# Performance work log

Measured on AMD Instinct MI355X. Metric: run time of the kernel, lower is better.

The kernel has to match this reference:

```python
import jax, jax.numpy as jnp
import numpy as np

B, T, C = 4, 2048, 2048
H, KV, HD = 16, 4, 128  # n_head, n_kv_head, head_dim
G = H // KV             # query heads per kv head


def _rope(t, cos, sin):
    # t: [B, T, h, HD]; cos/sin: [T, HD//2] -> broadcast as [1, T, 1, HD//2]
    tr = t.reshape(t.shape[:-1] + (HD // 2, 2))
    t_r, t_i = tr[..., 0], tr[..., 1]
    c = cos[None, :, None, :]
    s = sin[None, :, None, :]
    o_r = t_r * c - t_i * s
    o_i = t_r * s + t_i * c
    return jnp.stack((o_r, o_i), axis=-1).reshape(t.shape)


def setup_inputs() -> dict:
    key = jax.random.key(0)
    ks = jax.random.split(key, 7)
    sc = 0.02
    return {
        "x": jax.random.normal(ks[0], (B, T, C), jnp.float32),
        "cos_freqs": jnp.cos(jnp.outer(jnp.arange(T, dtype=jnp.float32),
                                       1.0 / (10000.0 ** (jnp.arange(HD // 2, dtype=jnp.float32) * 2 / HD)))),
        "sin_freqs": jnp.sin(jnp.outer(jnp.arange(T, dtype=jnp.float32),
                                       1.0 / (10000.0 ** (jnp.arange(HD // 2, dtype=jnp.float32) * 2 / HD)))),
        "wq": jax.random.normal(ks[1], (H * HD, C), jnp.float32) * sc,
        "wk": jax.random.normal(ks[2], (KV * HD, C), jnp.float32) * sc,
        "wv": jax.random.normal(ks[3], (KV * HD, C), jnp.float32) * sc,
        "wo": jax.random.normal(ks[4], (C, H * HD), jnp.float32) * sc,
    }


def reference(x, cos_freqs, sin_freqs, wq, wk, wv, wo):
    # projections (Linear with bias=False: y = x @ W.T)
    q = (x @ wq.T).reshape(B, T, H, HD)
    k = (x @ wk.T).reshape(B, T, KV, HD)
    v = (x @ wv.T).reshape(B, T, KV, HD)
    q, k = _rope(q, cos_freqs, sin_freqs), _rope(k, cos_freqs, sin_freqs)
    # GQA attention without materializing repeated K/V: group q heads per kv head
    qg = q.reshape(B, T, KV, G, HD).transpose(0, 2, 3, 1, 4)  # [B,KV,G,T,HD]
    kh = k.transpose(0, 2, 1, 3)                              # [B,KV,T,HD]
    vh = v.transpose(0, 2, 1, 3)                              # [B,KV,T,HD]
    scale = 1.0 / jnp.sqrt(jnp.float32(HD))
    scores = jnp.einsum('bkgtd,bksd->bkgts', qg, kh) * scale  # [B,KV,G,T,T]
    mask = jnp.tril(jnp.ones((T, T), dtype=bool))
    scores = jnp.where(mask, scores, jnp.float32(-jnp.inf))
    attn = jax.nn.softmax(scores, axis=-1)
    out = jnp.einsum('bkgts,bksd->bkgtd', attn, vh)           # [B,KV,G,T,HD]
    out = out.transpose(0, 3, 1, 2, 4).reshape(B, T, H * HD)
    return out @ wo.T
```

## Files before the change

### kernel.cpp

```cpp
#include <hip/hip_runtime.h>
#include <hip/hip_bf16.h>
#include <math.h>

typedef __attribute__((ext_vector_type(8))) short short8;
typedef __attribute__((ext_vector_type(4))) float floatx4;

__device__ __forceinline__ float bf2f(unsigned short u) {
  union { unsigned int i; float f; } x; x.i = ((unsigned int)u) << 16; return x.f;
}
__device__ __forceinline__ unsigned short f2bf(float f) {
  union { float f; unsigned int i; } x; x.f = f;
  unsigned int r = x.i + 0x7FFFu + ((x.i >> 16) & 1u);
  return (unsigned short)(r >> 16);
}
__device__ __forceinline__ unsigned int pack2bf(float a, float b) {
  return (unsigned int)f2bf(a) | ((unsigned int)f2bf(b) << 16);
}
__device__ __forceinline__ void gl16(const void* g, void* l) {
  __builtin_amdgcn_global_load_lds(
      (const __attribute__((address_space(1))) unsigned int*)g,
      (__attribute__((address_space(3))) unsigned int*)l, 16, 0, 0);
}
#define BARF  do { __builtin_amdgcn_s_barrier(); asm volatile("" ::: "memory"); } while (0)

__global__ void cvt_f32_bf16(const float* __restrict__ in, unsigned short* __restrict__ out, int n4) {
  int i = blockIdx.x * blockDim.x + threadIdx.x;
  if (i >= n4) return;
  float4 v = ((const float4*)in)[i];
  ushort4 o;
  o.x = f2bf(v.x); o.y = f2bf(v.y); o.z = f2bf(v.z); o.w = f2bf(v.w);
  ((ushort4*)out)[i] = o;
}

template<int MODE>
__global__ __launch_bounds__(512, 2) void gemm_bt(const unsigned short* __restrict__ A,
                                                  const unsigned short* __restrict__ Bw,
                                                  void* __restrict__ out0,
                                                  unsigned short* __restrict__ vtg,
                                                  int M, int N, int K, int nbx) {
  extern __shared__ unsigned short SM[];
  const int nb = gridDim.x;
  const int bid = blockIdx.x;
  const int tile = (bid & 7) * (nb >> 3) + (bid >> 3);
  const int n0 = (tile % nbx) * 256, m0 = (tile / nbx) * 256;
  const int tid = threadIdx.x;
  const int lane = tid & 63, wave = tid >> 6;
  const int wm = wave >> 2, wn = wave & 3;
  const int r = lane & 15, g = lane >> 4;
  const int rh = r >> 1;
  const int slot = (((r & 1) << 2) | g) ^ rh;

  const int sg8 = (tid & 7) ^ ((tid >> 3) & 7);
  const int srow = 2 * (tid >> 3) + (sg8 >> 2);
  const int scol = (sg8 & 3) * 8;
  const unsigned short* Agb = A  + (size_t)(m0 + srow) * K + scol;
  const unsigned short* Bgb = Bw + (size_t)(n0 + srow) * K + scol;
  const size_t K128 = (size_t)K * 128;
  char* const SMb = (char*)SM;

  const int aob = (wm * 64 + rh) * 64 + slot * 8;
  const int bob = 16384 + (wn * 32 + rh) * 64 + slot * 8;

  auto STA = [&](int s, int t, int kh) {
    const unsigned short* gp = Agb + ((size_t)t << 6) + kh * 32;
    char* d = SMb + s * 65536 + kh * 16384 + wave * 1024;
    gl16(gp,        d);
    gl16(gp + K128, d + 8192);
  };
  auto STB = [&](int s, int t, int kh) {
    const unsigned short* gp = Bgb + ((size_t)t << 6) + kh * 32;
    char* d = SMb + s * 65536 + 32768 + kh * 16384 + wave * 1024;
    gl16(gp,        d);
    gl16(gp + K128, d + 8192);
  };

  floatx4 acc[8][4] = {};
  const int NT = K >> 6;

  STA(0, 0, 0); STB(0, 0, 0);
  STA(0, 0, 1); STB(0, 0, 1);
  asm volatile("s_waitcnt vmcnt(4)" ::: "memory");
  BARF;

  for (int t = 0; t < NT; ++t) {
    const int s = t & 1;
    const unsigned short* Ls = SM + s * 32768;
    const bool pf = (t + 1 < NT);
    short8 bfr[4], af[4];

#pragma unroll
    for (int j = 0; j < 4; ++j) bfr[j] = *(const short8*)&Ls[bob + j * 512];
#pragma unroll
    for (int i = 0; i < 4; ++i) af[i] = *(const short8*)&Ls[aob + i * 512];
    if (pf) STA(s ^ 1, t + 1, 0);
    BARF;
    __builtin_amdgcn_s_setprio(1);
#pragma unroll
    for (int i = 0; i < 4; ++i)
#pragma unroll
      for (int j = 0; j < 4; ++j)
        acc[i][j] = __builtin_amdgcn_mfma_f32_16x16x32_bf16(af[i], bfr[j], acc[i][j], 0, 0, 0);
    __builtin_amdgcn_s_setprio(0);
    BARF;

#pragma unroll
    for (int i = 0; i < 4; ++i) af[i] = *(const short8*)&Ls[aob + (4 + i) * 512];
    if (pf) {
      STB(s ^ 1, t + 1, 0);
      asm volatile("s_waitcnt vmcnt(4)" ::: "memory");
    } else {
      asm volatile("s_waitcnt vmcnt(0)" ::: "memory");
    }
    BARF;
    __builtin_amdgcn_s_setprio(1);
#pragma unroll
    for (int i = 0; i < 4; ++i)
#pragma unroll
      for (int j = 0; j < 4; ++j)
        acc[4 + i][j] = __builtin_amdgcn_mfma_f32_16x16x32_bf16(af[i], bfr[j], acc[4 + i][j], 0, 0, 0);
    __builtin_amdgcn_s_setprio(0);
    BARF;

#pragma unroll
    for (int j = 0; j < 4; ++j) bfr[j] = *(const short8*)&Ls[bob + 8192 + j * 512];
#pragma unroll
    for (int i = 0; i < 4; ++i) af[i] = *(const short8*)&Ls[aob + 8192 + i * 512];
    if (pf) STA(s ^ 1, t + 1, 1);
    BARF;
    __builtin_amdgcn_s_setprio(1);
#pragma unroll
    for (int i = 0; i < 4; ++i)
#pragma unroll
      for (int j = 0; j < 4; ++j)
        acc[i][j] = __builtin_amdgcn_mfma_f32_16x16x32_bf16(af[i], bfr[j], acc[i][j], 0, 0, 0);
    __builtin_amdgcn_s_setprio(0);
    BARF;

#pragma unroll
    for (int i = 0; i < 4; ++i) af[i] = *(const short8*)&Ls[aob + 8192 + (4 + i) * 512];
    if (pf) {
      STB(s ^ 1, t + 1, 1);
      asm volatile("s_waitcnt vmcnt(4)" ::: "memory");
    }
    BARF;
    __builtin_amdgcn_s_setprio(1);
#pragma unroll
    for (int i = 0; i < 4; ++i)
#pragma unroll
      for (int j = 0; j < 4; ++j)
        acc[4 + i][j] = __builtin_amdgcn_mfma_f32_16x16x32_bf16(af[i], bfr[j], acc[4 + i][j], 0, 0, 0);
    __builtin_amdgcn_s_setprio(0);
    BARF;
  }

  if (MODE == 0) {
    float* SMf = (float*)SM;
    float* outp = (float*)out0;
#pragma unroll
    for (int sp = 0; sp < 4; ++sp) {
      __syncthreads();
      if (wn == sp) {
#pragma unroll
        for (int i = 0; i < 8; ++i)
#pragma unroll
          for (int j = 0; j < 4; ++j)
#pragma unroll
            for (int q = 0; q < 4; ++q)
              SMf[(wm * 128 + i * 16 + g * 4 + q) * 64 + j * 16 + r] = acc[i][j][q];
      }
      __syncthreads();
#pragma unroll
      for (int it = 0; it < 8; ++it) {
        int c = it * 512 + tid;
        int ml = c >> 4, c4 = c & 15;
        float4 v = *(float4*)&SMf[ml * 64 + c4 * 4];
        *(float4*)(outp + (size_t)(m0 + ml) * N + n0 + sp * 64 + c4 * 4) = v;
      }
    }
  } else if (n0 < 2560) {
    unsigned short* outp = (unsigned short*)out0;
#pragma unroll
    for (int sp = 0; sp < 2; ++sp) {
      __syncthreads();
      if (wm == sp) {
#pragma unroll
        for (int i = 0; i < 8; ++i)
#pragma unroll
          for (int j = 0; j < 4; ++j)
#pragma unroll
            for (int q = 0; q < 4; ++q)
              SM[(i * 16 + g * 4 + q) * 256 + wn * 64 + j * 16 + r] = f2bf(acc[i][j][q]);
      }
      __syncthreads();
#pragma unroll
      for (int it = 0; it < 8; ++it) {
        int c = it * 512 + tid;
        int ml = c >> 5, c8 = c & 31;
        short8 v = *(short8*)&SM[ml * 256 + c8 * 8];
        *(short8*)(outp + (size_t)(m0 + sp * 128 + ml) * N + n0 + c8 * 8) = v;
      }
    }
  } else {
#pragma unroll
    for (int sp = 0; sp < 8; ++sp) {
      __syncthreads();
      if (wave == sp) {
#pragma unroll
        for (int i = 0; i < 8; ++i)
#pragma unroll
          for (int j = 0; j < 4; ++j)
#pragma unroll
            for (int q = 0; q < 4; ++q) {
              int ml = i * 16 + g * 4 + q;
              int nl = j * 16 + r;
              SM[nl * 128 + (((ml >> 3) ^ (nl & 7)) << 3) + (ml & 7)] = f2bf(acc[i][j][q]);
            }
      }
      __syncthreads();
#pragma unroll
      for (int it = 0; it < 2; ++it) {
        int c = it * 512 + tid;
        int nl = c >> 4, m8 = c & 15;
        short8 v = *(short8*)&SM[nl * 128 + ((m8 ^ (nl & 7)) << 3)];
        *(short8*)(vtg + (size_t)(n0 - 2560 + (sp & 3) * 64 + nl) * 8192 + m0 + (sp >> 2) * 128 + m8 * 8) = v;
      }
    }
  }
}

__global__ void rope_inplace(unsigned short* __restrict__ t,
                             const float* __restrict__ cosf, const float* __restrict__ sinf,
                             int heads, int rowStride, int total, float scale) {
  int i = blockIdx.x * blockDim.x + threadIdx.x;
  if (i >= total) return;
  int d8 = i & 15;
  int rem = i >> 4;
  int head = rem % heads;
  int tok = rem / heads;
  int tpos = tok & 2047;
  unsigned short* p = t + (size_t)tok * rowStride + head * 128 + d8 * 8;
  short8 v = *(short8*)p;
  float4 c = *(const float4*)(cosf + (size_t)tpos * 64 + d8 * 4);
  float4 s = *(const float4*)(sinf + (size_t)tpos * 64 + d8 * 4);
  float cc[4] = {c.x, c.y, c.z, c.w};
  float ss[4] = {s.x, s.y, s.z, s.w};
  short8 o;
#pragma unroll
  for (int j = 0; j < 4; ++j) {
    float tr = bf2f((unsigned short)v[2 * j]);
    float ti = bf2f((unsigned short)v[2 * j + 1]);
    float orr = (tr * cc[j] - ti * ss[j]) * scale;
    float oi  = (tr * ss[j] + ti * cc[j]) * scale;
    o[2 * j]     = (short)f2bf(orr);
    o[2 * j + 1] = (short)f2bf(oi);
  }
  *(short8*)p = o;
}

__global__ __launch_bounds__(256, 2) void attn_fwd(const unsigned short* __restrict__ QKV,
                                                   const unsigned short* __restrict__ VT,
                                                   unsigned short* __restrict__ O) {
  constexpr int T = 2048;
  constexpr int LDQ = 3072;
  constexpr float NEG = -1e30f;
  __shared__ unsigned short Ks[2][64 * 128];
  __shared__ unsigned short Vs[2][128 * 64];
  const int gid = blockIdx.x;
  const int hb  = gid & 63;
  const int qb  = 15 - (gid >> 6);
  const int h = hb & 15, b = hb >> 4;
  const int kvh = h >> 2;
  const int tid = threadIdx.x, lane = tid & 63, w = tid >> 6;
  const int r = lane & 15, g = lane >> 4;
  const int rbase = (r & 3) + ((r >> 2) << 3);
  const int swzr  = (r & 3) | (((r >> 2) & 1) << 2);
  const size_t bT = (size_t)b * T;

  const unsigned short* Kgb = QKV + bT * LDQ + 2048 + kvh * 128;
  const unsigned short* Vgb = VT + (size_t)(kvh * 128) * 8192 + b * 2048;

  auto STAGE = [&](int bi, int kv0) {
#pragma unroll
    for (int t2 = 0; t2 < 4; ++t2) {
      int ck = w * 4 + t2;
      { int row = ck * 4 + (lane >> 4); int c16 = lane & 15;
        int swz = (row & 3) | (((row >> 3) & 1) << 2);
        gl16(Kgb + (size_t)(kv0 + row) * LDQ + ((c16 ^ swz) << 3),
             (char*)(&Ks[bi][0]) + ck * 1024); }
      { int row = ck * 8 + (lane >> 3); int c16 = lane & 7;
        gl16(Vgb + (size_t)row * 8192 + kv0 + ((c16 ^ (row & 7)) << 3),
             (char*)(&Vs[bi][0]) + ck * 1024); }
    }
  };

  const int q0 = qb * 128;

  short8 qf[2][4];
#pragma unroll
  for (int qt = 0; qt < 2; ++qt) {
    const unsigned short* qp = QKV + (bT + q0 + w * 32 + qt * 16 + r) * LDQ + h * 128;
#pragma unroll
    for (int c = 0; c < 4; ++c) qf[qt][c] = *(const short8*)(qp + c * 32 + g * 8);
  }

  floatx4 acc[8][2] = {};
  float mrun[2] = {NEG, NEG};
  float lrun[2] = {0.f, 0.f};

  const int ntiles = (q0 + 128) >> 6;
  STAGE(0, 0);
  asm volatile("s_waitcnt vmcnt(0)" ::: "memory");
  __syncthreads();

  for (int t = 0; t < ntiles; ++t) {
    const int cur = t & 1;
    const int kv0 = t << 6;
    if (t + 1 < ntiles) STAGE(cur ^ 1, (t + 1) << 6);

    if (kv0 <= q0 + w * 32 + 31) {
      floatx4 st[2][4] = {};
      __builtin_amdgcn_s_setprio(1);
#pragma unroll
      for (int c = 0; c < 4; ++c) {
        short8 kf[4];
#pragma unroll
        for (int kt = 0; kt < 4; ++kt) {
          const int row = rbase + ((kt & 1) << 2) + ((kt >> 1) << 5);
          kf[kt] = *(const short8*)&Ks[cur][row * 128 + (((g + 4 * c) ^ swzr) << 3)];
        }
#pragma unroll
        for (int qt = 0; qt < 2; ++qt)
#pragma unroll
          for (int kt = 0; kt < 4; ++kt)
            st[qt][kt] = __builtin_amdgcn_mfma_f32_16x16x32_bf16(kf[kt], qf[qt][c], st[qt][kt], 0, 0, 0);
      }
      __builtin_amdgcn_s_setprio(0);

      short8 va[2][8];
#pragma unroll
      for (int kc = 0; kc < 2; ++kc)
#pragma unroll
        for (int dt = 0; dt < 8; ++dt)
          va[kc][dt] = *(const short8*)&Vs[cur][(dt * 16 + r) * 64 + (((g + 4 * kc) ^ (r & 7)) << 3)];

#pragma unroll
      for (int qt = 0; qt < 2; ++qt) {
        const int qmin = q0 + w * 32 + qt * 16;
        const int qrow = qmin + r;
        float x[4][4];
        bool needmask = (kv0 + 64 > qmin);
#pragma unroll
        for (int kt = 0; kt < 4; ++kt) {
          const int kvb = kv0 + ((kt >> 1) << 5) + (g << 3) + ((kt & 1) << 2);
#pragma unroll
          for (int j = 0; j < 4; ++j) {
            float v = st[qt][kt][j];
            if (needmask) v = (kvb + j <= qrow) ? v : NEG;
            x[kt][j] = v;
          }
        }
        float mloc = x[0][0];
#pragma unroll
        for (int kt = 0; kt < 4; ++kt)
#pragma unroll
          for (int j = 0; j < 4; ++j) mloc = fmaxf(mloc, x[kt][j]);
        mloc = fmaxf(mloc, __shfl_xor(mloc, 16));
        mloc = fmaxf(mloc, __shfl_xor(mloc, 32));
        if (!__all(mloc <= mrun[qt] + 8.f)) {
          float mnew = fmaxf(mrun[qt], mloc);
          float al = __expf(mrun[qt] - mnew);
          mrun[qt] = mnew;
          lrun[qt] *= al;
#pragma unroll
          for (int dt = 0; dt < 8; ++dt) acc[dt][qt] *= al;
        }
        float pr[4][4], ssum = 0.f;
#pragma unroll
        for (int kt = 0; kt < 4; ++kt)
#pragma unroll
          for (int j = 0; j < 4; ++j) { pr[kt][j] = __expf(x[kt][j] - mrun[qt]); ssum += pr[kt][j]; }
        ssum += __shfl_xor(ssum, 16);
        ssum += __shfl_xor(ssum, 32);
        lrun[qt] += ssum;
        uint2 pk[4];
#pragma unroll
        for (int kt = 0; kt < 4; ++kt) {
          pk[kt].x = pack2bf(pr[kt][0], pr[kt][1]);
          pk[kt].y = pack2bf(pr[kt][2], pr[kt][3]);
        }
        __builtin_amdgcn_s_setprio(1);
#pragma unroll
        for (int kc = 0; kc < 2; ++kc) {
          union { unsigned int u[4]; short8 s; } bw;
          bw.u[0] = pk[2 * kc].x;
          bw.u[1] = pk[2 * kc].y;
          bw.u[2] = pk[2 * kc + 1].x;
          bw.u[3] = pk[2 * kc + 1].y;
#pragma unroll
          for (int dt = 0; dt < 8; ++dt)
            acc[dt][qt] = __builtin_amdgcn_mfma_f32_16x16x32_bf16(va[kc][dt], bw.s, acc[dt][qt], 0, 0, 0);
        }
        __builtin_amdgcn_s_setprio(0);
      }
    }

    asm volatile("s_waitcnt vmcnt(0)" ::: "memory");
    __syncthreads();
  }

#pragma unroll
  for (int qt = 0; qt < 2; ++qt) {
    float inv = 1.f / lrun[qt];
    unsigned short* op = O + (bT + q0 + w * 32 + qt * 16 + r) * 2048 + h * 128;
#pragma unroll
    for (int dt = 0; dt < 8; ++dt) {
      uint2 pkd;
      pkd.x = pack2bf(acc[dt][qt][0] * inv, acc[dt][qt][1] * inv);
      pkd.y = pack2bf(acc[dt][qt][2] * inv, acc[dt][qt][3] * inv);
      *(uint2*)(op + dt * 16 + g * 4) = pkd;
    }
  }
}

extern "C" void kernel_launch(void* const* d_in, const int* in_sizes, int n_in,
                              void* d_out, int out_size, void* d_ws, size_t ws_size,
                              hipStream_t stream) {
  const float* x    = (const float*)d_in[0];
  const float* cosf = (const float*)d_in[1];
  const float* sinf = (const float*)d_in[2];
  const float* wq   = (const float*)d_in[3];
  const float* wk   = (const float*)d_in[4];
  const float* wv   = (const float*)d_in[5];
  const float* wo   = (const float*)d_in[6];

  unsigned short* xb   = (unsigned short*)d_ws;
  unsigned short* qkvw = xb   + 16777216;
  unsigned short* wob  = qkvw + 6291456;
  unsigned short* qkv  = wob  + 4194304;
  unsigned short* Vtg  = qkv  + 25165824;
  unsigned short* AO   = Vtg  + 4194304;

  static int _attr_once = []() {
    hipFuncSetAttribute((const void*)gemm_bt<0>, hipFuncAttributeMaxDynamicSharedMemorySize, 131072);
    hipFuncSetAttribute((const void*)gemm_bt<1>, hipFuncAttributeMaxDynamicSharedMemorySize, 131072);
    return 0;
  }();
  (void)_attr_once;

  cvt_f32_bf16<<<16384, 256, 0, stream>>>(x,  xb,  4194304);
  cvt_f32_bf16<<<4096,  256, 0, stream>>>(wq, qkvw,           1048576);
  cvt_f32_bf16<<<1024,  256, 0, stream>>>(wk, qkvw + 4194304, 262144);
  cvt_f32_bf16<<<1024,  256, 0, stream>>>(wv, qkvw + 5242880, 262144);
  cvt_f32_bf16<<<4096,  256, 0, stream>>>(wo, wob, 1048576);

  gemm_bt<1><<<384, 512, 131072, stream>>>(xb, qkvw, qkv, Vtg, 8192, 3072, 2048, 12);

  rope_inplace<<<8192, 256, 0, stream>>>(qkv,        cosf, sinf, 16, 3072, 2097152, 0.08838834764831845f);
  rope_inplace<<<2048, 256, 0, stream>>>(qkv + 2048, cosf, sinf, 4,  3072, 524288,  1.0f);

  attn_fwd<<<1024, 256, 0, stream>>>(qkv, Vtg, AO);

  gemm_bt<0><<<256, 512, 131072, stream>>>(AO, wob, d_out, nullptr, 8192, 2048, 2048, 8);
}
```

Measured before the change: 367.6 us.

## Software-pipeline GEMM LDS fragment loads and cut per-iteration barriers to one

Restructures the GEMM main loop so register fragments for the next subtile are loaded from LDS while MFMAs on the current fragments run. It also prefetches the first fragments of the next K tile after a single end-of-iteration barrier. Eight barriers per iteration become one, and the global-to-LDS prefetches for A and B are issued together. In exchange it uses more vector registers for the double-buffered fragments and waits for all outstanding global loads (vmcnt(0)) at the end of each iteration instead of allowing partial overlap.

Result: no change. 361.6 us (-1.6%).

```diff
diff --git a/kernel.cpp b/kernel.cpp
--- a/kernel.cpp
+++ b/kernel.cpp
@@ -79,78 +79,74 @@
 
   STA(0, 0, 0); STB(0, 0, 0);
   STA(0, 0, 1); STB(0, 0, 1);
-  asm volatile("s_waitcnt vmcnt(4)" ::: "memory");
-  BARF;
+  asm volatile("s_waitcnt vmcnt(0)" ::: "memory");
+  __builtin_amdgcn_s_barrier();
+  asm volatile("" ::: "memory");
+
+  short8 bfrA[4], afA[4];
+#pragma unroll
+  for (int j = 0; j < 4; ++j) bfrA[j] = *(const short8*)&SM[bob + j * 512];
+#pragma unroll
+  for (int i = 0; i < 4; ++i) afA[i] = *(const short8*)&SM[aob + i * 512];
 
   for (int t = 0; t < NT; ++t) {
     const int s = t & 1;
     const unsigned short* Ls = SM + s * 32768;
+    const unsigned short* Ln = SM + (s ^ 1) * 32768;
     const bool pf = (t + 1 < NT);
-    short8 bfr[4], af[4];
-
-#pragma unroll
-    for (int j = 0; j < 4; ++j) bfr[j] = *(const short8*)&Ls[bob + j * 512];
-#pragma unroll
-    for (int i = 0; i < 4; ++i) af[i] = *(const short8*)&Ls[aob + i * 512];
-    if (pf) STA(s ^ 1, t + 1, 0);
-    BARF;
+    short8 afB[4], bfrB[4], afA2[4], afB2[4];
+
+#pragma unroll
+    for (int i = 0; i < 4; ++i) afB[i] = *(const short8*)&Ls[aob + (4 + i) * 512];
+    if (pf) { STA(s ^ 1, t + 1, 0); STB(s ^ 1, t + 1, 0); }
     __builtin_amdgcn_s_setprio(1);
 #pragma unroll
     for (int i = 0; i < 4; ++i)
 #pragma unroll
       for (int j = 0; j < 4; ++j)
-        acc[i][j] = __builtin_amdgcn_mfma_f32_16x16x32_bf16(af[i], bfr[j], acc[i][j], 0, 0, 0);
+        acc[i][j] = __builtin_amdgcn_mfma_f32_16x16x32_bf16(afA[i], bfrA[j], acc[i][j], 0, 0, 0);
     __builtin_amdgcn_s_setprio(0);
-    BARF;
-
-#pragma unroll
-    for (int i = 0; i < 4; ++i) af[i] = *(const short8*)&Ls[aob + (4 + i) * 512];
+
+#pragma unroll
+    for (int j = 0; j < 4; ++j) bfrB[j] = *(const short8*)&Ls[bob + 8192 + j * 512];
+#pragma unroll
+    for (int i = 0; i < 4; ++i) afA2[i] = *(const short8*)&Ls[aob + 8192 + i * 512];
+    if (pf) { STA(s ^ 1, t + 1, 1); STB(s ^ 1, t + 1, 1); }
+    __builtin_amdgcn_s_setprio(1);
+#pragma unroll
+    for (int i = 0; i < 4; ++i)
+#pragma unroll
+      for (int j = 0; j < 4; ++j)
+        acc[4 + i][j] = __builtin_amdgcn_mfma_f32_16x16x32_bf16(afB[i], bfrA[j], acc[4 + i][j], 0, 0, 0);
+    __builtin_amdgcn_s_setprio(0);
+
+#pragma unroll
+    for (int i = 0; i < 4; ++i) afB2[i] = *(const short8*)&Ls[aob + 8192 + (4 + i) * 512];
+    __builtin_amdgcn_s_setprio(1);
+#pragma unroll
+    for (int i = 0; i < 4; ++i)
+#pragma unroll
+      for (int j = 0; j < 4; ++j)
+        acc[i][j] = __builtin_amdgcn_mfma_f32_16x16x32_bf16(afA2[i], bfrB[j], acc[i][j], 0, 0, 0);
+    __builtin_amdgcn_s_setprio(0);
+
+    asm volatile("s_waitcnt lgkmcnt(0)" ::: "memory");
+    if (pf) asm volatile("s_waitcnt vmcnt(0)" ::: "memory");
+    __builtin_amdgcn_s_barrier();
+    asm volatile("" ::: "memory");
     if (pf) {
-      STB(s ^ 1, t + 1, 0);
-      asm volatile("s_waitcnt vmcnt(4)" ::: "memory");
-    } else {
-      asm volatile("s_waitcnt vmcnt(0)" ::: "memory");
-    }
-    BARF;
+#pragma unroll
+      for (int j = 0; j < 4; ++j) bfrA[j] = *(const short8*)&Ln[bob + j * 512];
+#pragma unroll
+      for (int i = 0; i < 4; ++i) afA[i] = *(const short8*)&Ln[aob + i * 512];
+    }
     __builtin_amdgcn_s_setprio(1);
 #pragma unroll
     for (int i = 0; i < 4; ++i)
 #pragma unroll
       for (int j = 0; j < 4; ++j)
-        acc[4 + i][j] = __builtin_amdgcn_mfma_f32_16x16x32_bf16(af[i], bfr[j], acc[4 + i][j], 0, 0, 0);
+        acc[4 + i][j] = __builtin_amdgcn_mfma_f32_16x16x32_bf16(afB2[i], bfrB[j], acc[4 + i][j], 0, 0, 0);
     __builtin_amdgcn_s_setprio(0);
-    BARF;
-
-#pragma unroll
-    for (int j = 0; j < 4; ++j) bfr[j] = *(const short8*)&Ls[bob + 8192 + j * 512];
-#pragma unroll
-    for (int i = 0; i < 4; ++i) af[i] = *(const short8*)&Ls[aob + 8192 + i * 512];
-    if (pf) STA(s ^ 1, t + 1, 1);
-    BARF;
-    __builtin_amdgcn_s_setprio(1);
-#pragma unroll
-    for (int i = 0; i < 4; ++i)
-#pragma unroll
-      for (int j = 0; j < 4; ++j)
-        acc[i][j] = __builtin_amdgcn_mfma_f32_16x16x32_bf16(af[i], bfr[j], acc[i][j], 0, 0, 0);
-    __builtin_amdgcn_s_setprio(0);
-    BARF;
-
-#pragma unroll
-    for (int i = 0; i < 4; ++i) af[i] = *(const short8*)&Ls[aob + 8192 + (4 + i) * 512];
-    if (pf) {
-      STB(s ^ 1, t + 1, 1);
-      asm volatile("s_waitcnt vmcnt(4)" ::: "memory");
-    }
-    BARF;
-    __builtin_amdgcn_s_setprio(1);
-#pragma unroll
-    for (int i = 0; i < 4; ++i)
-#pragma unroll
-      for (int j = 0; j < 4; ++j)
-        acc[4 + i][j] = __builtin_amdgcn_mfma_f32_16x16x32_bf16(af[i], bfr[j], acc[4 + i][j], 0, 0, 0);
-    __builtin_amdgcn_s_setprio(0);
-    BARF;
   }
 
   if (MODE == 0) {
```
